# Optimization experiments

Measured on AMD Instinct MI355X. Metric: run time of the kernel, lower is better.

Reference implementation:

```python
import jax, jax.numpy as jnp
import numpy as np


def _ln(x, g, eps=1e-5):
    # channel LayerNorm over dim 1, unbiased=False variance
    mean = jnp.mean(x, axis=1, keepdims=True)
    var = jnp.mean((x - mean) ** 2, axis=1, keepdims=True)
    return (x - mean) * jax.lax.rsqrt(var + eps) * g


def _c11(x, w, b):
    # 1x1 conv: w (O,C), b (O,)
    return jnp.einsum('bchw,oc->bohw', x, w) + b[None, :, None, None]


def _dw(x, w, b):
    # depthwise 3x3 conv, SAME padding; w (C,1,3,3), b (C,)
    C = x.shape[1]
    y = jax.lax.conv_general_dilated(x, w, (1, 1), 'SAME',
                                     feature_group_count=C,
                                     dimension_numbers=('NCHW', 'OIHW', 'NCHW'))
    return y + b[None, :, None, None]


def _forward(F_i, F_w, g1, g2, qw1, qb1, kw1, kb1, vw1, vb1,
             qw2, qb2, kw2, kb2, vw2, vb2,
             qdw1, qdb1, kdw1, kdb1, vdw1, vdb1,
             qdw2, qdb2, kdw2, kdb2, vdw2, vdb2, lw, lb):
    B, C1, H, W = F_i.shape
    C2 = F_w.shape[1]
    HW = H * W
    fi = _ln(F_i, g1)
    fw = _ln(F_w, g2)
    # qkv = 1x1 conv -> depthwise conv; then RAW C-order reshape (torch .view)
    Qi = _dw(_c11(fi, qw1, qb1), qdw1, qdb1).reshape(B, HW, C1)
    Ki = _dw(_c11(fi, kw1, kb1), kdw1, kdb1).reshape(B, HW, C1)
    Vi = _dw(_c11(fi, vw1, vb1), vdw1, vdb1).reshape(B, C1, HW)
    Qw = _dw(_c11(fw, qw2, qb2), qdw2, qdb2).reshape(B, HW, C2)
    Kw = _dw(_c11(fw, kw2, kb2), kdw2, kdb2).reshape(B, HW, C2)
    Vw = _dw(_c11(fw, vw2, vb2), vdw2, vdb2).reshape(B, C2, HW)
    # channel cross-attention: (B,C1,HW)@(B,HW,C2) -> (B,C1,C2)
    a1 = jax.nn.softmax(jnp.einsum('bnc,bnd->bcd', Qi, Kw), axis=-1)
    a2 = jax.nn.softmax(jnp.einsum('bnc,bnd->bcd', Qw, Ki), axis=-1)
    Aw = jnp.einsum('bcd,bdn->bcn', a1, Vw).reshape(B, H, W, C2).transpose(0, 3, 1, 2)
    Ai = jnp.einsum('bcd,bdn->bcn', a2, Vi).reshape(B, H, W, C1).transpose(0, 3, 1, 2)
    cat = jnp.concatenate([Aw, Ai], axis=1)  # (B, C2+C1, H, W)
    Ct = cat.shape[1]
    flat = cat.reshape(B, Ct, HW).transpose(0, 2, 1).reshape(-1, Ct)  # (B*HW, Ct)
    out = flat @ lw.T + lb  # (B*HW, Cout)
    Cout = lb.shape[0]
    # faithful replication of torch's view/permute/view tail
    out = out.reshape(B, Cout, H, W).transpose(0, 2, 3, 1).reshape(B, Cout, H, W)
    return out + F_i + F_w


def setup_inputs() -> dict:
    key = jax.random.key(0)
    ks = jax.random.split(key, 20)
    B, C, H, W = 8, 128, 128, 128
    d = {}
    d['F_i'] = jax.random.normal(ks[0], (B, C, H, W), jnp.float32)
    d['F_w'] = jax.random.normal(ks[1], (B, C, H, W), jnp.float32)
    d['g1'] = jnp.ones((1, C, 1, 1), jnp.float32)
    d['g2'] = jnp.ones((1, C, 1, 1), jnp.float32)
    s = 1.0 / np.sqrt(C)
    i = 2
    for n in ['qw1', 'kw1', 'vw1', 'qw2', 'kw2', 'vw2']:
        d[n] = jax.random.normal(ks[i], (C, C), jnp.float32) * s
        i += 1
    for n in ['qb1', 'kb1', 'vb1', 'qb2', 'kb2', 'vb2']:
        d[n] = jnp.zeros((C,), jnp.float32)
    sd = 1.0 / 3.0
    for n in ['qdw1', 'kdw1', 'vdw1', 'qdw2', 'kdw2', 'vdw2']:
        d[n] = jax.random.normal(ks[i], (C, 1, 3, 3), jnp.float32) * sd
        i += 1
    for n in ['qdb1', 'kdb1', 'vdb1', 'qdb2', 'kdb2', 'vdb2']:
        d[n] = jnp.zeros((C,), jnp.float32)
    d['lw'] = jax.random.normal(ks[i], (C, 2 * C), jnp.float32) * (1.0 / np.sqrt(2 * C))
    d['lb'] = jnp.zeros((C,), jnp.float32)
    return d


def reference(F_i, F_w, g1, g2, qw1, qb1, kw1, kb1, vw1, vb1,
              qw2, qb2, kw2, kb2, vw2, vb2,
              qdw1, qdb1, kdw1, kdb1, vdw1, vdb1,
              qdw2, qdb2, kdw2, kdb2, vdw2, vdb2, lw, lb):
    return _forward(F_i, F_w, g1, g2, qw1, qb1, kw1, kb1, vw1, vb1,
                    qw2, qb2, kw2, kb2, vw2, vb2,
                    qdw1, qdb1, kdw1, kdb1, vdw1, vdb1,
                    qdw2, qdb2, kdw2, kdb2, vdw2, vdb2, lw, lb)
```

## Files before the change

kernel.cpp:

```cpp
#include <hip/hip_runtime.h>
#include <cstddef>
#include <cstring>

#define HW 16384
#define CC 128
#define NB 8
#define GB 4

typedef short bf16x8_t __attribute__((ext_vector_type(8)));
typedef float floatx4 __attribute__((ext_vector_type(4)));

__device__ inline unsigned short f2bf(float f) {
  unsigned u; __builtin_memcpy(&u, &f, 4);
  u += 0x7fffu + ((u >> 16) & 1u);
  return (unsigned short)(u >> 16);
}
__device__ inline float bf2f(unsigned short s) {
  unsigned u = ((unsigned)s) << 16; float f; __builtin_memcpy(&f, &u, 4);
  return f;
}

__global__ __launch_bounds__(256) void k_ln_stats(const float* __restrict__ x,
                                                  float* __restrict__ mean,
                                                  float* __restrict__ rstd) {
  int idx = blockIdx.x * 256 + threadIdx.x;
  int b = idx >> 14;
  int p = idx & (HW - 1);
  const float* xp = x + ((size_t)b << 21) + p;
  float s = 0.f, ss = 0.f;
  for (int c = 0; c < CC; ++c) {
    float v = xp[(size_t)c << 14];
    s += v;
    ss += v * v;
  }
  float m = s * (1.0f / CC);
  float var = ss * (1.0f / CC) - m * m;
  mean[idx] = m;
  rstd[idx] = rsqrtf(var + 1e-5f);
}

__global__ __launch_bounds__(256) void k_conv1x1_mfma(
    const float* __restrict__ X, const float* __restrict__ W,
    const float* __restrict__ bias, const float* __restrict__ g,
    const float* __restrict__ mean, const float* __restrict__ rstd,
    float* __restrict__ Y, int b0) {
  __shared__ __align__(16) float raw[32][132];
  __shared__ __align__(16) short Ah[128][40];
  __shared__ __align__(16) short Al[128][40];
  __shared__ __align__(16) short Bh[128][40];
  __shared__ __align__(16) short Bl[128][40];
  const int bl = blockIdx.y;
  const int b = b0 + bl;
  const int p0 = blockIdx.x * 128;
  const int t = threadIdx.x;
  const int lane = t & 63, wv = t >> 6;
  const int quad = lane >> 4, l15 = lane & 15;
  const int wr = wv >> 1, wc = wv & 1;

  const int s1c = t >> 3, s1p = (t & 7) * 16;
  const int sao = t >> 1, sas = (t & 1) * 16;
  const int s2p = t & 127, s2o = t >> 7;
  const float mu = mean[b * HW + p0 + s2p];
  const float rs = rstd[b * HW + p0 + s2p];

  const float* Xb = X + ((size_t)b << 21);
  floatx4 acc[4][4];
#pragma unroll
  for (int i = 0; i < 4; ++i)
#pragma unroll
    for (int j = 0; j < 4; ++j) acc[i][j] = (floatx4){0.f, 0.f, 0.f, 0.f};

  for (int k0 = 0; k0 < 128; k0 += 32) {
    {
      const float* xp = Xb + ((size_t)(k0 + s1c) << 14) + p0 + s1p;
#pragma unroll
      for (int u = 0; u < 4; ++u)
        *reinterpret_cast<float4*>(&raw[s1c][s1p + 4 * u]) =
            *reinterpret_cast<const float4*>(xp + 4 * u);
    }
    {
      const float* wp = W + sao * 128 + k0 + sas;
      const float* gp = g + k0 + sas;
      short th[16], tl[16];
#pragma unroll
      for (int j = 0; j < 16; ++j) {
        float v = wp[j] * gp[j];
        unsigned short h = f2bf(v);
        th[j] = (short)h;
        tl[j] = (short)f2bf(v - bf2f(h));
      }
#pragma unroll
      for (int j = 0; j < 2; ++j) {
        *reinterpret_cast<bf16x8_t*>(&Ah[sao][sas + 8 * j]) =
            *reinterpret_cast<bf16x8_t*>(&th[8 * j]);
        *reinterpret_cast<bf16x8_t*>(&Al[sao][sas + 8 * j]) =
            *reinterpret_cast<bf16x8_t*>(&tl[8 * j]);
      }
    }
    __syncthreads();
#pragma unroll
    for (int item = 0; item < 2; ++item) {
      const int oct = s2o + 2 * item;
      short th[8], tl[8];
#pragma unroll
      for (int jj = 0; jj < 8; ++jj) {
        float v = (raw[oct * 8 + jj][s2p] - mu) * rs;
        unsigned short h = f2bf(v);
        th[jj] = (short)h;
        tl[jj] = (short)f2bf(v - bf2f(h));
      }
      *reinterpret_cast<bf16x8_t*>(&Bh[s2p][oct * 8]) =
          *reinterpret_cast<bf16x8_t*>(&th[0]);
      *reinterpret_cast<bf16x8_t*>(&Bl[s2p][oct * 8]) =
          *reinterpret_cast<bf16x8_t*>(&tl[0]);
    }
    __syncthreads();
    bf16x8_t afh[4], afl[4], bfh[4], bfl[4];
#pragma unroll
    for (int i = 0; i < 4; ++i) {
      const int m = wr * 64 + i * 16 + l15;
      afh[i] = *reinterpret_cast<const bf16x8_t*>(&Ah[m][quad * 8]);
      afl[i] = *reinterpret_cast<const bf16x8_t*>(&Al[m][quad * 8]);
    }
#pragma unroll
    for (int j = 0; j < 4; ++j) {
      const int p = wc * 64 + j * 16 + l15;
      bfh[j] = *reinterpret_cast<const bf16x8_t*>(&Bh[p][quad * 8]);
      bfl[j] = *reinterpret_cast<const bf16x8_t*>(&Bl[p][quad * 8]);
    }
#pragma unroll
    for (int i = 0; i < 4; ++i)
#pragma unroll
      for (int j = 0; j < 4; ++j) {
        acc[i][j] = __builtin_amdgcn_mfma_f32_16x16x32_bf16(afh[i], bfh[j], acc[i][j], 0, 0, 0);
        acc[i][j] = __builtin_amdgcn_mfma_f32_16x16x32_bf16(afh[i], bfl[j], acc[i][j], 0, 0, 0);
        acc[i][j] = __builtin_amdgcn_mfma_f32_16x16x32_bf16(afl[i], bfh[j], acc[i][j], 0, 0, 0);
      }
    __syncthreads();
  }
  float* Yb = Y + ((size_t)bl << 21);
#pragma unroll
  for (int i = 0; i < 4; ++i) {
#pragma unroll
    for (int j = 0; j < 4; ++j) {
#pragma unroll
      for (int r = 0; r < 4; ++r) {
        const int o = wr * 64 + i * 16 + quad * 4 + r;
        const int p = p0 + wc * 64 + j * 16 + l15;
        Yb[((size_t)o << 14) + p] = acc[i][j][r] + bias[o];
      }
    }
  }
}

__global__ __launch_bounds__(256) void k_score_mfma(
    const float* __restrict__ Yq, const float* __restrict__ Yk,
    const float* __restrict__ qdw, const float* __restrict__ qdb,
    const float* __restrict__ kdw, const float* __restrict__ kdb,
    float* __restrict__ P) {
  __shared__ __align__(16) float raw[32][132];
  __shared__ __align__(16) short Ah[128][40];
  __shared__ __align__(16) short Al[128][40];
  __shared__ __align__(16) short Bh[128][40];
  __shared__ __align__(16) short Bl[128][40];
  const int ch = blockIdx.x;
  const int bl = blockIdx.y;
  const int t = threadIdx.x;
  const int lane = t & 63, wv = t >> 6;
  const int quad = lane >> 4, l15 = lane & 15;
  const int wr = wv >> 1, wc = wv & 1;
  const int h_loc = t >> 3;
  const int w0 = (t & 7) * 16;
  const int s2w = t & 127, s2o = t >> 7;
  const int cc = ch;
  const float* Yqb = Yq + ((size_t)bl << 21) + ((size_t)cc << 14);
  const float* Ykb = Yk + ((size_t)bl << 21) + ((size_t)cc << 14);
  const float* qwt = qdw + cc * 9;
  const float* kwt = kdw + cc * 9;
  const float qbv = qdb[cc], kbv = kdb[cc];

  floatx4 acc[4][4];
#pragma unroll
  for (int i = 0; i < 4; ++i)
#pragma unroll
    for (int j = 0; j < 4; ++j) acc[i][j] = (floatx4){0.f, 0.f, 0.f, 0.f};

  for (int k0 = 0; k0 < 128; k0 += 32) {
    const int h = k0 + h_loc;
#pragma unroll
    for (int side = 0; side < 2; ++side) {
      const float* Yc = side ? Ykb : Yqb;
      const float* wt = side ? kwt : qwt;
      const float bias = side ? kbv : qbv;
      float a[16];
#pragma unroll
      for (int j = 0; j < 16; ++j) a[j] = bias;
#pragma unroll
      for (int dy = 0; dy < 3; ++dy) {
        const int hh = h + dy - 1;
        if (hh < 0 || hh > 127) continue;
        const float* rp = Yc + (hh << 7) + w0;
        float4 f0 = *reinterpret_cast<const float4*>(rp);
        float4 f1 = *reinterpret_cast<const float4*>(rp + 4);
        float4 f2 = *reinterpret_cast<const float4*>(rp + 8);
        float4 f3 = *reinterpret_cast<const float4*>(rp + 12);
        float s[18];
        s[1] = f0.x;  s[2] = f0.y;  s[3] = f0.z;  s[4] = f0.w;
        s[5] = f1.x;  s[6] = f1.y;  s[7] = f1.z;  s[8] = f1.w;
        s[9] = f2.x;  s[10] = f2.y; s[11] = f2.z; s[12] = f2.w;
        s[13] = f3.x; s[14] = f3.y; s[15] = f3.z; s[16] = f3.w;
        s[0] = (w0 > 0) ? rp[-1] : 0.f;
        s[17] = (w0 < 112) ? rp[16] : 0.f;
        const float wa = wt[dy * 3 + 0], wb = wt[dy * 3 + 1], wc2 = wt[dy * 3 + 2];
#pragma unroll
        for (int j = 0; j < 16; ++j)
          a[j] = fmaf(s[j], wa, fmaf(s[j + 1], wb, fmaf(s[j + 2], wc2, a[j])));
      }
#pragma unroll
      for (int u = 0; u < 4; ++u)
        *reinterpret_cast<float4*>(&raw[h_loc][w0 + 4 * u]) =
            (float4){a[4 * u], a[4 * u + 1], a[4 * u + 2], a[4 * u + 3]};
      __syncthreads();
      short* dh = side ? &Bh[0][0] : &Ah[0][0];
      short* dl = side ? &Bl[0][0] : &Al[0][0];
#pragma unroll
      for (int item = 0; item < 2; ++item) {
        const int oct = s2o + 2 * item;
        short th[8], tl[8];
#pragma unroll
        for (int jj = 0; jj < 8; ++jj) {
          float v = raw[oct * 8 + jj][s2w];
          unsigned short hb = f2bf(v);
          th[jj] = (short)hb;
          tl[jj] = (short)f2bf(v - bf2f(hb));
        }
        *reinterpret_cast<bf16x8_t*>(&dh[s2w * 40 + oct * 8]) =
            *reinterpret_cast<bf16x8_t*>(&th[0]);
        *reinterpret_cast<bf16x8_t*>(&dl[s2w * 40 + oct * 8]) =
            *reinterpret_cast<bf16x8_t*>(&tl[0]);
      }
      __syncthreads();
    }
    bf16x8_t afh[4], afl[4], bfh[4], bfl[4];
#pragma unroll
    for (int i = 0; i < 4; ++i) {
      const int m = wr * 64 + i * 16 + l15;
      afh[i] = *reinterpret_cast<const bf16x8_t*>(&Ah[m][quad * 8]);
      afl[i] = *reinterpret_cast<const bf16x8_t*>(&Al[m][quad * 8]);
    }
#pragma unroll
    for (int j = 0; j < 4; ++j) {
      const int n = wc * 64 + j * 16 + l15;
      bfh[j] = *reinterpret_cast<const bf16x8_t*>(&Bh[n][quad * 8]);
      bfl[j] = *reinterpret_cast<const bf16x8_t*>(&Bl[n][quad * 8]);
    }
#pragma unroll
    for (int i = 0; i < 4; ++i)
#pragma unroll
      for (int j = 0; j < 4; ++j) {
        acc[i][j] = __builtin_amdgcn_mfma_f32_16x16x32_bf16(afh[i], bfh[j], acc[i][j], 0, 0, 0);
        acc[i][j] = __builtin_amdgcn_mfma_f32_16x16x32_bf16(afh[i], bfl[j], acc[i][j], 0, 0, 0);
        acc[i][j] = __builtin_amdgcn_mfma_f32_16x16x32_bf16(afl[i], bfh[j], acc[i][j], 0, 0, 0);
      }
  }
  float* Pp = P + ((size_t)(ch * GB + bl) << 14);
#pragma unroll
  for (int i = 0; i < 4; ++i) {
#pragma unroll
    for (int j = 0; j < 4; ++j) {
#pragma unroll
      for (int r = 0; r < 4; ++r) {
        const int c = wr * 64 + i * 16 + quad * 4 + r;
        const int d = wc * 64 + j * 16 + l15;
        Pp[c * 128 + d] = acc[i][j][r];
      }
    }
  }
}

__global__ __launch_bounds__(256) void k_score_reduce(const float* __restrict__ P,
                                                      float* __restrict__ S) {
  int idx = blockIdx.x * 256 + threadIdx.x;
  int bl = idx >> 14;
  int rem = idx & 16383;
  float s = 0.f;
  for (int c = 0; c < 128; ++c) s += P[((size_t)(c * GB + bl) << 14) + rem];
  S[idx] = s;
}

__global__ __launch_bounds__(128) void k_softmax(float* __restrict__ S) {
  __shared__ float red[128];
  const int row = blockIdx.x;
  const int t = threadIdx.x;
  float v = S[row * 128 + t];
  red[t] = v;
  __syncthreads();
  for (int s = 64; s > 0; s >>= 1) {
    if (t < s) red[t] = fmaxf(red[t], red[t + s]);
    __syncthreads();
  }
  float mx = red[0];
  __syncthreads();
  float e = expf(v - mx);
  red[t] = e;
  __syncthreads();
  for (int s = 64; s > 0; s >>= 1) {
    if (t < s) red[t] += red[t + s];
    __syncthreads();
  }
  S[row * 128 + t] = e / red[0];
}

__global__ __launch_bounds__(256) void k_dw_t(const float* __restrict__ Y,
                                              const float* __restrict__ Kw,
                                              const float* __restrict__ db,
                                              unsigned short* __restrict__ Vt) {
  __shared__ unsigned short T[128][33];
  const int h = blockIdx.x;
  const int c0 = blockIdx.y * 32;
  const int bl = blockIdx.z;
  const int t = threadIdx.x;
  const int cl = t >> 3;
  const int w0 = (t & 7) * 16;
  const int c = c0 + cl;
  const float* Yc = Y + ((size_t)bl << 21) + ((size_t)c << 14);
  const float* wt = Kw + c * 9;
  float a[16];
#pragma unroll
  for (int j = 0; j < 16; ++j) a[j] = db[c];
#pragma unroll
  for (int dy = 0; dy < 3; ++dy) {
    const int hh = h + dy - 1;
    if (hh < 0 || hh > 127) continue;
    const float* rp = Yc + (hh << 7) + w0;
    float4 f0 = *reinterpret_cast<const float4*>(rp);
    float4 f1 = *reinterpret_cast<const float4*>(rp + 4);
    float4 f2 = *reinterpret_cast<const float4*>(rp + 8);
    float4 f3 = *reinterpret_cast<const float4*>(rp + 12);
    float s[18];
    s[1] = f0.x;  s[2] = f0.y;  s[3] = f0.z;  s[4] = f0.w;
    s[5] = f1.x;  s[6] = f1.y;  s[7] = f1.z;  s[8] = f1.w;
    s[9] = f2.x;  s[10] = f2.y; s[11] = f2.z; s[12] = f2.w;
    s[13] = f3.x; s[14] = f3.y; s[15] = f3.z; s[16] = f3.w;
    s[0] = (w0 > 0) ? rp[-1] : 0.f;
    s[17] = (w0 < 112) ? rp[16] : 0.f;
    const float wa = wt[dy * 3 + 0], wb = wt[dy * 3 + 1], wc2 = wt[dy * 3 + 2];
#pragma unroll
    for (int j = 0; j < 16; ++j)
      a[j] = fmaf(s[j], wa, fmaf(s[j + 1], wb, fmaf(s[j + 2], wc2, a[j])));
  }
#pragma unroll
  for (int j = 0; j < 16; ++j) T[w0 + j][cl] = f2bf(a[j]);
  __syncthreads();
  const int w = t >> 1, half = t & 1;
  unsigned short tmp[16];
#pragma unroll
  for (int j = 0; j < 16; ++j) tmp[j] = T[w][half * 16 + j];
  uint4 v0, v1;
  unsigned* vp0 = reinterpret_cast<unsigned*>(&v0);
  unsigned* vp1 = reinterpret_cast<unsigned*>(&v1);
#pragma unroll
  for (int j = 0; j < 4; ++j) {
    vp0[j] = (unsigned)tmp[2 * j] | ((unsigned)tmp[2 * j + 1] << 16);
    vp1[j] = (unsigned)tmp[8 + 2 * j] | ((unsigned)tmp[8 + 2 * j + 1] << 16);
  }
  unsigned short* dst = Vt + ((size_t)bl << 21) + ((size_t)((h << 7) + w) << 7)
                        + c0 + half * 16;
  *reinterpret_cast<uint4*>(dst) = v0;
  *reinterpret_cast<uint4*>(dst + 8) = v1;
}

__global__ __launch_bounds__(256) void k_av_mfma(
    const float* __restrict__ S, const unsigned short* __restrict__ Vt,
    unsigned short* __restrict__ O) {
  __shared__ __align__(16) short As[128][136];
  const int bl = blockIdx.y;
  const int p0 = blockIdx.x * 128;
  const int t = threadIdx.x;
  const int lane = t & 63, wv = t >> 6;
  const int quad = lane >> 4, l15 = lane & 15;
  const int wr = wv >> 1, wc = wv & 1;
  {
    const float* Ab = S + ((size_t)bl << 14);
    const int r = t >> 1, hf = (t & 1) * 64;
    const float* src = Ab + r * 128 + hf;
    short tmp[64];
#pragma unroll
    for (int j = 0; j < 64; ++j) tmp[j] = (short)f2bf(src[j]);
#pragma unroll
    for (int j = 0; j < 8; ++j)
      *reinterpret_cast<bf16x8_t*>(&As[r][hf + j * 8]) =
          *reinterpret_cast<bf16x8_t*>(&tmp[j * 8]);
  }
  __syncthreads();
  floatx4 acc[4][4];
#pragma unroll
  for (int i = 0; i < 4; ++i)
#pragma unroll
    for (int j = 0; j < 4; ++j) acc[i][j] = (floatx4){0.f, 0.f, 0.f, 0.f};
  const unsigned short* Vb = Vt + ((size_t)bl << 21);
#pragma unroll
  for (int d0 = 0; d0 < 128; d0 += 32) {
    bf16x8_t af[4], bf[4];
#pragma unroll
    for (int i = 0; i < 4; ++i) {
      const int m = wr * 64 + i * 16 + l15;
      af[i] = *reinterpret_cast<const bf16x8_t*>(&As[m][d0 + quad * 8]);
    }
#pragma unroll
    for (int j = 0; j < 4; ++j) {
      const int p = p0 + wc * 64 + j * 16 + l15;
      bf[j] = *reinterpret_cast<const bf16x8_t*>(Vb + ((size_t)p << 7) + d0 + quad * 8);
    }
#pragma unroll
    for (int i = 0; i < 4; ++i)
#pragma unroll
      for (int j = 0; j < 4; ++j)
        acc[i][j] = __builtin_amdgcn_mfma_f32_16x16x32_bf16(af[i], bf[j], acc[i][j], 0, 0, 0);
  }
  unsigned short* Ob = O + ((size_t)bl << 21);
#pragma unroll
  for (int i = 0; i < 4; ++i) {
#pragma unroll
    for (int j = 0; j < 4; ++j) {
#pragma unroll
      for (int r = 0; r < 4; ++r) {
        const int c = wr * 64 + i * 16 + quad * 4 + r;
        const int p = p0 + wc * 64 + j * 16 + l15;
        Ob[((size_t)c << 14) + p] = f2bf(acc[i][j][r]);
      }
    }
  }
}

__global__ __launch_bounds__(256) void k_final2_mfma(
    const unsigned short* __restrict__ A1, const unsigned short* __restrict__ A2,
    const float* __restrict__ lw, const float* __restrict__ lb,
    const float* __restrict__ Fi, const float* __restrict__ Fw,
    float* __restrict__ out, int b0) {
  __shared__ __align__(16) short As[128][136];
  const int c2 = blockIdx.x;
  const int bl = blockIdx.y;
  const int b = b0 + bl;
  const int t = threadIdx.x;
  const int lane = t & 63, wv = t >> 6;
  const int quad = lane >> 4, l15 = lane & 15;
  const int wr = wv >> 1, wc = wv & 1;
  floatx4 acc[4][4];
#pragma unroll
  for (int i = 0; i < 4; ++i)
#pragma unroll
    for (int j = 0; j < 4; ++j) acc[i][j] = (floatx4){0.f, 0.f, 0.f, 0.f};
#pragma unroll
  for (int phase = 0; phase < 2; ++phase) {
    {
      const int r = t >> 1, hf = (t & 1) * 64;
      const float* src = lw + r * 256 + phase * 128 + hf;
      short tmp[64];
#pragma unroll
      for (int j = 0; j < 64; ++j) tmp[j] = (short)f2bf(src[j]);
#pragma unroll
      for (int j = 0; j < 8; ++j)
        *reinterpret_cast<bf16x8_t*>(&As[r][hf + j * 8]) =
            *reinterpret_cast<bf16x8_t*>(&tmp[j * 8]);
    }
    __syncthreads();
    const unsigned short* Ub = (phase ? A2 : A1) + ((size_t)bl << 21) + c2 * 128;
#pragma unroll
    for (int d0 = 0; d0 < 128; d0 += 32) {
      bf16x8_t af[4], bf[4];
#pragma unroll
      for (int i = 0; i < 4; ++i) {
        const int m = wr * 64 + i * 16 + l15;
        af[i] = *reinterpret_cast<const bf16x8_t*>(&As[m][d0 + quad * 8]);
      }
#pragma unroll
      for (int j = 0; j < 4; ++j) {
        const int n = wc * 64 + j * 16 + l15;
        bf[j] = *reinterpret_cast<const bf16x8_t*>(Ub + ((size_t)n << 14) + d0 + quad * 8);
      }
#pragma unroll
      for (int i = 0; i < 4; ++i)
#pragma unroll
        for (int j = 0; j < 4; ++j)
          acc[i][j] = __builtin_amdgcn_mfma_f32_16x16x32_bf16(af[i], bf[j], acc[i][j], 0, 0, 0);
    }
    __syncthreads();
  }
  const size_t obase = ((size_t)b << 21) + ((size_t)c2 << 14);
#pragma unroll
  for (int i = 0; i < 4; ++i) {
#pragma unroll
    for (int j = 0; j < 4; ++j) {
#pragma unroll
      for (int r = 0; r < 4; ++r) {
        const int h2 = wr * 64 + i * 16 + quad * 4 + r;
        const int w2 = wc * 64 + j * 16 + l15;
        const size_t a = obase + ((size_t)h2 << 7) + w2;
        out[a] = acc[i][j][r] + lb[h2] + Fi[a] + Fw[a];
      }
    }
  }
}

extern "C" void kernel_launch(void* const* d_in, const int* in_sizes, int n_in,
                              void* d_out, int out_size, void* d_ws, size_t ws_size,
                              hipStream_t stream) {
  const float* F_i  = (const float*)d_in[0];
  const float* F_w  = (const float*)d_in[1];
  const float* g1   = (const float*)d_in[2];
  const float* g2   = (const float*)d_in[3];
  const float* qw1  = (const float*)d_in[4];
  const float* kw1  = (const float*)d_in[5];
  const float* vw1  = (const float*)d_in[6];
  const float* qw2  = (const float*)d_in[7];
  const float* kw2  = (const float*)d_in[8];
  const float* vw2  = (const float*)d_in[9];
  const float* qb1  = (const float*)d_in[10];
  const float* kb1  = (const float*)d_in[11];
  const float* vb1  = (const float*)d_in[12];
  const float* qb2  = (const float*)d_in[13];
  const float* kb2  = (const float*)d_in[14];
  const float* vb2  = (const float*)d_in[15];
  const float* qdw1 = (const float*)d_in[16];
  const float* kdw1 = (const float*)d_in[17];
  const float* vdw1 = (const float*)d_in[18];
  const float* qdw2 = (const float*)d_in[19];
  const float* kdw2 = (const float*)d_in[20];
  const float* vdw2 = (const float*)d_in[21];
  const float* qdb1 = (const float*)d_in[22];
  const float* kdb1 = (const float*)d_in[23];
  const float* vdb1 = (const float*)d_in[24];
  const float* qdb2 = (const float*)d_in[25];
  const float* kdb2 = (const float*)d_in[26];
  const float* vdb2 = (const float*)d_in[27];
  const float* lw   = (const float*)d_in[28];
  const float* lb   = (const float*)d_in[29];
  float* out = (float*)d_out;

  char* w = (char*)d_ws;
  const size_t NTOT = (size_t)NB * HW;
  float* meanI = (float*)w; w += NTOT * 4;
  float* rstdI = (float*)w; w += NTOT * 4;
  float* meanW = (float*)w; w += NTOT * 4;
  float* rstdW = (float*)w; w += NTOT * 4;
  float* S     = (float*)w; w += (size_t)GB * HW * 4;
  float* P     = (float*)w; w += (size_t)128 * GB * HW * 4;
  float* Yq    = (float*)w; w += ((size_t)GB << 21) * 4;
  char*  Ykreg = w;         w += ((size_t)GB << 21) * 4;
  float* Yk    = (float*)Ykreg;
  unsigned short* Vt = (unsigned short*)Ykreg;
  unsigned short* A2 = (unsigned short*)(Ykreg + ((size_t)GB << 21) * 2);
  unsigned short* A1 = (unsigned short*)w; w += ((size_t)GB << 21) * 2;

  dim3 blk(256);
  k_ln_stats<<<dim3(512), blk, 0, stream>>>(F_i, meanI, rstdI);
  k_ln_stats<<<dim3(512), blk, 0, stream>>>(F_w, meanW, rstdW);

  for (int b0 = 0; b0 < NB; b0 += GB) {
    k_conv1x1_mfma<<<dim3(128, GB), blk, 0, stream>>>(F_i, qw1, qb1, g1, meanI, rstdI, Yq, b0);
    k_conv1x1_mfma<<<dim3(128, GB), blk, 0, stream>>>(F_w, kw2, kb2, g2, meanW, rstdW, Yk, b0);
    k_score_mfma<<<dim3(128, GB), blk, 0, stream>>>(Yq, Yk, qdw1, qdb1, kdw2, kdb2, P);
    k_score_reduce<<<dim3(GB * HW / 256), blk, 0, stream>>>(P, S);
    k_softmax<<<dim3(GB * 128), dim3(128), 0, stream>>>(S);
    k_conv1x1_mfma<<<dim3(128, GB), blk, 0, stream>>>(F_w, vw2, vb2, g2, meanW, rstdW, Yq, b0);
    k_dw_t<<<dim3(128, 4, GB), blk, 0, stream>>>(Yq, vdw2, vdb2, Vt);
    k_av_mfma<<<dim3(128, GB), blk, 0, stream>>>(S, Vt, A1);

    k_conv1x1_mfma<<<dim3(128, GB), blk, 0, stream>>>(F_w, qw2, qb2, g2, meanW, rstdW, Yq, b0);
    k_conv1x1_mfma<<<dim3(128, GB), blk, 0, stream>>>(F_i, kw1, kb1, g1, meanI, rstdI, Yk, b0);
    k_score_mfma<<<dim3(128, GB), blk, 0, stream>>>(Yq, Yk, qdw2, qdb2, kdw1, kdb1, P);
    k_score_reduce<<<dim3(GB * HW / 256), blk, 0, stream>>>(P, S);
    k_softmax<<<dim3(GB * 128), dim3(128), 0, stream>>>(S);
    k_conv1x1_mfma<<<dim3(128, GB), blk, 0, stream>>>(F_i, vw1, vb1, g1, meanI, rstdI, Yq, b0);
    k_dw_t<<<dim3(128, 4, GB), blk, 0, stream>>>(Yq, vdw1, vdb1, Vt);
    k_av_mfma<<<dim3(128, GB), blk, 0, stream>>>(S, Vt, A2);

    k_final2_mfma<<<dim3(128, GB), blk, 0, stream>>>(A1, A2, lw, lb, F_i, F_w, out, b0);
  }
}
```

Before: 838.9 us.

## Precompute split-bf16 weights once and read MFMA A-operands from global

A new kernel converts the six gamma-scaled 1x1 conv weights into hi/lo bf16 pairs and the linear weight into bf16, once per call. The conv1x1 and final kernels then read these A fragments straight from global memory instead of converting them into shared memory in every block. k_av and k_final also halve their tile width to double the grid and drop their shared-memory staging. k_score shrinks its raw buffer and processes 16-row sub-tiles, which adds extra barriers. The cost is that A fragments are now fetched from global or L2 by every wave, with no shared-memory reuse.

Result: slower. 893.1 us (+6.5%).

```diff
diff --git a/kernel.cpp b/kernel.cpp
--- a/kernel.cpp
+++ b/kernel.cpp
@@ -39,16 +39,46 @@
   rstd[idx] = rsqrtf(var + 1e-5f);
 }
 
+__global__ __launch_bounds__(256) void k_wsplit(
+    const float* __restrict__ qw1, const float* __restrict__ kw2,
+    const float* __restrict__ vw2, const float* __restrict__ qw2,
+    const float* __restrict__ kw1, const float* __restrict__ vw1,
+    const float* __restrict__ g1, const float* __restrict__ g2,
+    const float* __restrict__ lw, unsigned short* __restrict__ whl,
+    unsigned short* __restrict__ lwh) {
+  int idx = blockIdx.x * 256 + threadIdx.x;
+  if (idx < 98304) {
+    const int set = idx >> 14;
+    const int e = idx & 16383;
+    const int c = e & 127;
+    const float* W; const float* g;
+    switch (set) {
+      case 0: W = qw1; g = g1; break;
+      case 1: W = kw2; g = g2; break;
+      case 2: W = vw2; g = g2; break;
+      case 3: W = qw2; g = g2; break;
+      case 4: W = kw1; g = g1; break;
+      default: W = vw1; g = g1; break;
+    }
+    float v = W[e] * g[c];
+    unsigned short h = f2bf(v);
+    whl[set * 32768 + e] = h;
+    whl[set * 32768 + 16384 + e] = f2bf(v - bf2f(h));
+  } else {
+    int e2 = idx - 98304;
+    lwh[e2] = f2bf(lw[e2]);
+  }
+}
+
 __global__ __launch_bounds__(256) void k_conv1x1_mfma(
-    const float* __restrict__ X, const float* __restrict__ W,
-    const float* __restrict__ bias, const float* __restrict__ g,
+    const float* __restrict__ X, const unsigned short* __restrict__ Wh,
+    const float* __restrict__ bias,
     const float* __restrict__ mean, const float* __restrict__ rstd,
     float* __restrict__ Y, int b0) {
   __shared__ __align__(16) float raw[32][132];
-  __shared__ __align__(16) short Ah[128][40];
-  __shared__ __align__(16) short Al[128][40];
   __shared__ __align__(16) short Bh[128][40];
   __shared__ __align__(16) short Bl[128][40];
+  const unsigned short* Wl = Wh + 16384;
   const int bl = blockIdx.y;
   const int b = b0 + bl;
   const int p0 = blockIdx.x * 128;
@@ -58,7 +88,6 @@
   const int wr = wv >> 1, wc = wv & 1;
 
   const int s1c = t >> 3, s1p = (t & 7) * 16;
-  const int sao = t >> 1, sas = (t & 1) * 16;
   const int s2p = t & 127, s2o = t >> 7;
   const float mu = mean[b * HW + p0 + s2p];
   const float rs = rstd[b * HW + p0 + s2p];
@@ -77,25 +106,6 @@
       for (int u = 0; u < 4; ++u)
         *reinterpret_cast<float4*>(&raw[s1c][s1p + 4 * u]) =
             *reinterpret_cast<const float4*>(xp + 4 * u);
-    }
-    {
-      const float* wp = W + sao * 128 + k0 + sas;
-      const float* gp = g + k0 + sas;
-      short th[16], tl[16];
-#pragma unroll
-      for (int j = 0; j < 16; ++j) {
-        float v = wp[j] * gp[j];
-        unsigned short h = f2bf(v);
-        th[j] = (short)h;
-        tl[j] = (short)f2bf(v - bf2f(h));
-      }
-#pragma unroll
-      for (int j = 0; j < 2; ++j) {
-        *reinterpret_cast<bf16x8_t*>(&Ah[sao][sas + 8 * j]) =
-            *reinterpret_cast<bf16x8_t*>(&th[8 * j]);
-        *reinterpret_cast<bf16x8_t*>(&Al[sao][sas + 8 * j]) =
-            *reinterpret_cast<bf16x8_t*>(&tl[8 * j]);
-      }
     }
     __syncthreads();
 #pragma unroll
@@ -119,8 +129,9 @@
 #pragma unroll
     for (int i = 0; i < 4; ++i) {
       const int m = wr * 64 + i * 16 + l15;
-      afh[i] = *reinterpret_cast<const bf16x8_t*>(&Ah[m][quad * 8]);
-      afl[i] = *reinterpret_cast<const bf16x8_t*>(&Al[m][quad * 8]);
+      const unsigned short* wp = Wh + m * 128 + k0 + quad * 8;
+      afh[i] = *reinterpret_cast<const bf16x8_t*>(wp);
+      afl[i] = *reinterpret_cast<const bf16x8_t*>(Wl + m * 128 + k0 + quad * 8);
     }
 #pragma unroll
     for (int j = 0; j < 4; ++j) {
@@ -158,7 +169,7 @@
     const float* __restrict__ qdw, const float* __restrict__ qdb,
     const float* __restrict__ kdw, const float* __restrict__ kdb,
     float* __restrict__ P) {
-  __shared__ __align__(16) float raw[32][132];
+  __shared__ __align__(16) float raw[16][132];
   __shared__ __align__(16) short Ah[128][40];
   __shared__ __align__(16) short Al[128][40];
   __shared__ __align__(16) short Bh[128][40];
@@ -169,8 +180,8 @@
   const int lane = t & 63, wv = t >> 6;
   const int quad = lane >> 4, l15 = lane & 15;
   const int wr = wv >> 1, wc = wv & 1;
-  const int h_loc = t >> 3;
-  const int w0 = (t & 7) * 16;
+  const int hl = t >> 4;
+  const int w0 = (t & 15) * 8;
   const int s2w = t & 127, s2o = t >> 7;
   const int cc = ch;
   const float* Yqb = Yq + ((size_t)bl << 21) + ((size_t)cc << 14);
@@ -186,60 +197,53 @@
     for (int j = 0; j < 4; ++j) acc[i][j] = (floatx4){0.f, 0.f, 0.f, 0.f};
 
   for (int k0 = 0; k0 < 128; k0 += 32) {
-    const int h = k0 + h_loc;
 #pragma unroll
     for (int side = 0; side < 2; ++side) {
       const float* Yc = side ? Ykb : Yqb;
       const float* wt = side ? kwt : qwt;
       const float bias = side ? kbv : qbv;
-      float a[16];
-#pragma unroll
-      for (int j = 0; j < 16; ++j) a[j] = bias;
-#pragma unroll
-      for (int dy = 0; dy < 3; ++dy) {
-        const int hh = h + dy - 1;
-        if (hh < 0 || hh > 127) continue;
-        const float* rp = Yc + (hh << 7) + w0;
-        float4 f0 = *reinterpret_cast<const float4*>(rp);
-        float4 f1 = *reinterpret_cast<const float4*>(rp + 4);
-        float4 f2 = *reinterpret_cast<const float4*>(rp + 8);
-        float4 f3 = *reinterpret_cast<const float4*>(rp + 12);
-        float s[18];
-        s[1] = f0.x;  s[2] = f0.y;  s[3] = f0.z;  s[4] = f0.w;
-        s[5] = f1.x;  s[6] = f1.y;  s[7] = f1.z;  s[8] = f1.w;
-        s[9] = f2.x;  s[10] = f2.y; s[11] = f2.z; s[12] = f2.w;
-        s[13] = f3.x; s[14] = f3.y; s[15] = f3.z; s[16] = f3.w;
-        s[0] = (w0 > 0) ? rp[-1] : 0.f;
-        s[17] = (w0 < 112) ? rp[16] : 0.f;
-        const float wa = wt[dy * 3 + 0], wb = wt[dy * 3 + 1], wc2 = wt[dy * 3 + 2];
-#pragma unroll
-        for (int j = 0; j < 16; ++j)
-          a[j] = fmaf(s[j], wa, fmaf(s[j + 1], wb, fmaf(s[j + 2], wc2, a[j])));
-      }
-#pragma unroll
-      for (int u = 0; u < 4; ++u)
-        *reinterpret_cast<float4*>(&raw[h_loc][w0 + 4 * u]) =
-            (float4){a[4 * u], a[4 * u + 1], a[4 * u + 2], a[4 * u + 3]};
-      __syncthreads();
       short* dh = side ? &Bh[0][0] : &Ah[0][0];
       short* dl = side ? &Bl[0][0] : &Al[0][0];
 #pragma unroll
-      for (int item = 0; item < 2; ++item) {
-        const int oct = s2o + 2 * item;
+      for (int sub = 0; sub < 2; ++sub) {
+        const int h = k0 + sub * 16 + hl;
+        float a[8];
+#pragma unroll
+        for (int j = 0; j < 8; ++j) a[j] = bias;
+#pragma unroll
+        for (int dy = 0; dy < 3; ++dy) {
+          const int hh = h + dy - 1;
+          if (hh < 0 || hh > 127) continue;
+          const float* rp = Yc + (hh << 7) + w0;
+          float4 f0 = *reinterpret_cast<const float4*>(rp);
+          float4 f1 = *reinterpret_cast<const float4*>(rp + 4);
+          float v[10];
+          v[0] = (w0 > 0) ? rp[-1] : 0.f;
+          v[1] = f0.x; v[2] = f0.y; v[3] = f0.z; v[4] = f0.w;
+          v[5] = f1.x; v[6] = f1.y; v[7] = f1.z; v[8] = f1.w;
+          v[9] = (w0 < 120) ? rp[8] : 0.f;
+          const float wa = wt[dy * 3 + 0], wb = wt[dy * 3 + 1], wc2 = wt[dy * 3 + 2];
+#pragma unroll
+          for (int j = 0; j < 8; ++j)
+            a[j] = fmaf(v[j], wa, fmaf(v[j + 1], wb, fmaf(v[j + 2], wc2, a[j])));
+        }
+        *reinterpret_cast<float4*>(&raw[hl][w0]) = (float4){a[0], a[1], a[2], a[3]};
+        *reinterpret_cast<float4*>(&raw[hl][w0 + 4]) = (float4){a[4], a[5], a[6], a[7]};
+        __syncthreads();
         short th[8], tl[8];
 #pragma unroll
         for (int jj = 0; jj < 8; ++jj) {
-          float v = raw[oct * 8 + jj][s2w];
+          float v = raw[s2o * 8 + jj][s2w];
           unsigned short hb = f2bf(v);
           th[jj] = (short)hb;
           tl[jj] = (short)f2bf(v - bf2f(hb));
         }
-        *reinterpret_cast<bf16x8_t*>(&dh[s2w * 40 + oct * 8]) =
+        *reinterpret_cast<bf16x8_t*>(&dh[s2w * 40 + sub * 16 + s2o * 8]) =
             *reinterpret_cast<bf16x8_t*>(&th[0]);
-        *reinterpret_cast<bf16x8_t*>(&dl[s2w * 40 + oct * 8]) =
+        *reinterpret_cast<bf16x8_t*>(&dl[s2w * 40 + sub * 16 + s2o * 8]) =
             *reinterpret_cast<bf16x8_t*>(&tl[0]);
-      }
-      __syncthreads();
+        __syncthreads();
+      }
     }
     bf16x8_t afh[4], afl[4], bfh[4], bfl[4];
 #pragma unroll
@@ -373,60 +377,55 @@
 __global__ __launch_bounds__(256) void k_av_mfma(
     const float* __restrict__ S, const unsigned short* __restrict__ Vt,
     unsigned short* __restrict__ O) {
-  __shared__ __align__(16) short As[128][136];
   const int bl = blockIdx.y;
-  const int p0 = blockIdx.x * 128;
+  const int p0 = blockIdx.x * 64;
   const int t = threadIdx.x;
   const int lane = t & 63, wv = t >> 6;
   const int quad = lane >> 4, l15 = lane & 15;
   const int wr = wv >> 1, wc = wv & 1;
-  {
-    const float* Ab = S + ((size_t)bl << 14);
-    const int r = t >> 1, hf = (t & 1) * 64;
-    const float* src = Ab + r * 128 + hf;
-    short tmp[64];
-#pragma unroll
-    for (int j = 0; j < 64; ++j) tmp[j] = (short)f2bf(src[j]);
-#pragma unroll
-    for (int j = 0; j < 8; ++j)
-      *reinterpret_cast<bf16x8_t*>(&As[r][hf + j * 8]) =
-          *reinterpret_cast<bf16x8_t*>(&tmp[j * 8]);
-  }
-  __syncthreads();
-  floatx4 acc[4][4];
+  const float* Sb = S + ((size_t)bl << 14);
+  floatx4 acc[4][2];
 #pragma unroll
   for (int i = 0; i < 4; ++i)
 #pragma unroll
-    for (int j = 0; j < 4; ++j) acc[i][j] = (floatx4){0.f, 0.f, 0.f, 0.f};
+    for (int j = 0; j < 2; ++j) acc[i][j] = (floatx4){0.f, 0.f, 0.f, 0.f};
   const unsigned short* Vb = Vt + ((size_t)bl << 21);
 #pragma unroll
   for (int d0 = 0; d0 < 128; d0 += 32) {
-    bf16x8_t af[4], bf[4];
+    bf16x8_t af[4], bf[2];
 #pragma unroll
     for (int i = 0; i < 4; ++i) {
       const int m = wr * 64 + i * 16 + l15;
-      af[i] = *reinterpret_cast<const bf16x8_t*>(&As[m][d0 + quad * 8]);
-    }
-#pragma unroll
-    for (int j = 0; j < 4; ++j) {
-      const int p = p0 + wc * 64 + j * 16 + l15;
+      const float* sp = Sb + m * 128 + d0 + quad * 8;
+      float4 x0 = *reinterpret_cast<const float4*>(sp);
+      float4 x1 = *reinterpret_cast<const float4*>(sp + 4);
+      short tmp[8];
+      tmp[0] = (short)f2bf(x0.x); tmp[1] = (short)f2bf(x0.y);
+      tmp[2] = (short)f2bf(x0.z); tmp[3] = (short)f2bf(x0.w);
+      tmp[4] = (short)f2bf(x1.x); tmp[5] = (short)f2bf(x1.y);
+      tmp[6] = (short)f2bf(x1.z); tmp[7] = (short)f2bf(x1.w);
+      af[i] = *reinterpret_cast<bf16x8_t*>(&tmp[0]);
+    }
+#pragma unroll
+    for (int j = 0; j < 2; ++j) {
+      const int p = p0 + wc * 32 + j * 16 + l15;
       bf[j] = *reinterpret_cast<const bf16x8_t*>(Vb + ((size_t)p << 7) + d0 + quad * 8);
     }
 #pragma unroll
     for (int i = 0; i < 4; ++i)
 #pragma unroll
-      for (int j = 0; j < 4; ++j)
+      for (int j = 0; j < 2; ++j)
         acc[i][j] = __builtin_amdgcn_mfma_f32_16x16x32_bf16(af[i], bf[j], acc[i][j], 0, 0, 0);
   }
   unsigned short* Ob = O + ((size_t)bl << 21);
 #pragma unroll
   for (int i = 0; i < 4; ++i) {
 #pragma unroll
-    for (int j = 0; j < 4; ++j) {
+    for (int j = 0; j < 2; ++j) {
 #pragma unroll
       for (int r = 0; r < 4; ++r) {
         const int c = wr * 64 + i * 16 + quad * 4 + r;
-        const int p = p0 + wc * 64 + j * 16 + l15;
+        const int p = p0 + wc * 32 + j * 16 + l15;
         Ob[((size_t)c << 14) + p] = f2bf(acc[i][j][r]);
       }
     }
@@ -435,67 +434,55 @@
 
 __global__ __launch_bounds__(256) void k_final2_mfma(
     const unsigned short* __restrict__ A1, const unsigned short* __restrict__ A2,
-    const float* __restrict__ lw, const float* __restrict__ lb,
+    const unsigned short* __restrict__ lwh, const float* __restrict__ lb,
     const float* __restrict__ Fi, const float* __restrict__ Fw,
     float* __restrict__ out, int b0) {
-  __shared__ __align__(16) short As[128][136];
   const int c2 = blockIdx.x;
   const int bl = blockIdx.y;
+  const int nb = blockIdx.z * 64;
   const int b = b0 + bl;
   const int t = threadIdx.x;
   const int lane = t & 63, wv = t >> 6;
   const int quad = lane >> 4, l15 = lane & 15;
   const int wr = wv >> 1, wc = wv & 1;
-  floatx4 acc[4][4];
+  floatx4 acc[4][2];
 #pragma unroll
   for (int i = 0; i < 4; ++i)
 #pragma unroll
-    for (int j = 0; j < 4; ++j) acc[i][j] = (floatx4){0.f, 0.f, 0.f, 0.f};
+    for (int j = 0; j < 2; ++j) acc[i][j] = (floatx4){0.f, 0.f, 0.f, 0.f};
 #pragma unroll
   for (int phase = 0; phase < 2; ++phase) {
-    {
-      const int r = t >> 1, hf = (t & 1) * 64;
-      const float* src = lw + r * 256 + phase * 128 + hf;
-      short tmp[64];
-#pragma unroll
-      for (int j = 0; j < 64; ++j) tmp[j] = (short)f2bf(src[j]);
-#pragma unroll
-      for (int j = 0; j < 8; ++j)
-        *reinterpret_cast<bf16x8_t*>(&As[r][hf + j * 8]) =
-            *reinterpret_cast<bf16x8_t*>(&tmp[j * 8]);
-    }
-    __syncthreads();
     const unsigned short* Ub = (phase ? A2 : A1) + ((size_t)bl << 21) + c2 * 128;
 #pragma unroll
     for (int d0 = 0; d0 < 128; d0 += 32) {
-      bf16x8_t af[4], bf[4];
+      bf16x8_t af[4], bf[2];
 #pragma unroll
       for (int i = 0; i < 4; ++i) {
         const int m = wr * 64 + i * 16 + l15;
-        af[i] = *reinterpret_cast<const bf16x8_t*>(&As[m][d0 + quad * 8]);
-      }
-#pragma unroll
-      for (int j = 0; j < 4; ++j) {
-        const int n = wc * 64 + j * 16 + l15;
+        af[i] = *reinterpret_cast<const bf16x8_t*>(
+            lwh + m * 256 + phase * 128 + d0 + quad * 8);
+      }
+#pragma unroll
+      for (int j = 0; j < 2; ++j) {
+        const int n = nb + wc * 32 + j * 16 + l15;
         bf[j] = *reinterpret_cast<const bf16x8_t*>(Ub + ((size_t)n << 14) + d0 + quad * 8);
       }
 #pragma unroll
       for (int i = 0; i < 4; ++i)
 #pragma unroll
-        for (int j = 0; j < 4; ++j)
+        for (int j = 0; j < 2; ++j)
           acc[i][j] = __builtin_amdgcn_mfma_f32_16x16x32_bf16(af[i], bf[j], acc[i][j], 0, 0, 0);
     }
-    __syncthreads();
   }
   const size_t obase = ((size_t)b << 21) + ((size_t)c2 << 14);
 #pragma unroll
   for (int i = 0; i < 4; ++i) {
 #pragma unroll
-    for (int j = 0; j < 4; ++j) {
+    for (int j = 0; j < 2; ++j) {
 #pragma unroll
       for (int r = 0; r < 4; ++r) {
         const int h2 = wr * 64 + i * 16 + quad * 4 + r;
-        const int w2 = wc * 64 + j * 16 + l15;
+        const int w2 = nb + wc * 32 + j * 16 + l15;
         const size_t a = obase + ((size_t)h2 << 7) + w2;
         out[a] = acc[i][j][r] + lb[h2] + Fi[a] + Fw[a];
       }
@@ -545,6 +532,8 @@
   float* meanW = (float*)w; w += NTOT * 4;
   float* rstdW = (float*)w; w += NTOT * 4;
   float* S     = (float*)w; w += (size_t)GB * HW * 4;
+  unsigned short* whl = (unsigned short*)w; w += 6 * 32768 * 2;
+  unsigned short* lwh = (unsigned short*)w; w += 32768 * 2;
   float* P     = (float*)w; w += (size_t)128 * GB * HW * 4;
   float* Yq    = (float*)w; w += ((size_t)GB << 21) * 4;
   char*  Ykreg = w;         w += ((size_t)GB << 21) * 4;
@@ -556,26 +545,34 @@
   dim3 blk(256);
   k_ln_stats<<<dim3(512), blk, 0, stream>>>(F_i, meanI, rstdI);
   k_ln_stats<<<dim3(512), blk, 0, stream>>>(F_w, meanW, rstdW);
+  k_wsplit<<<dim3(512), blk, 0, stream>>>(qw1, kw2, vw2, qw2, kw1, vw1,
+                                          g1, g2, lw, whl, lwh);
+  const unsigned short* wQ1 = whl;
+  const unsigned short* wK2 = whl + 32768;
+  const unsigned short* wV2 = whl + 65536;
+  const unsigned short* wQ2 = whl + 98304;
+  const unsigned short* wK1 = whl + 131072;
+  const unsigned short* wV1 = whl + 163840;
 
   for (int b0 = 0; b0 < NB; b0 += GB) {
-    k_conv1x1_mfma<<<dim3(128, GB), blk, 0, stream>>>(F_i, qw1, qb1, g1, meanI, rstdI, Yq, b0);
-    k_conv1x1_mfma<<<dim3(128, GB), blk, 0, stream>>>(F_w, kw2, kb2, g2, meanW, rstdW, Yk, b0);
+    k_conv1x1_mfma<<<dim3(128, GB), blk, 0, stream>>>(F_i, wQ1, qb1, meanI, rstdI, Yq, b0);
+    k_conv1x1_mfma<<<dim3(128, GB), blk, 0, stream>>>(F_w, wK2, kb2, meanW, rstdW, Yk, b0);
     k_score_mfma<<<dim3(128, GB), blk, 0, stream>>>(Yq, Yk, qdw1, qdb1, kdw2, kdb2, P);
     k_score_reduce<<<dim3(GB * HW / 256), blk, 0, stream>>>(P, S);
     k_softmax<<<dim3(GB * 128), dim3(128), 0, stream>>>(S);
-    k_conv1x1_mfma<<<dim3(128, GB), blk, 0, stream>>>(F_w, vw2, vb2, g2, meanW, rstdW, Yq, b0);
+    k_conv1x1_mfma<<<dim3(128, GB), blk, 0, stream>>>(F_w, wV2, vb2, meanW, rstdW, Yq, b0);
     k_dw_t<<<dim3(128, 4, GB), blk, 0, stream>>>(Yq, vdw2, vdb2, Vt);
-    k_av_mfma<<<dim3(128, GB), blk, 0, stream>>>(S, Vt, A1);
-
-    k_conv1x1_mfma<<<dim3(128, GB), blk, 0, stream>>>(F_w, qw2, qb2, g2, meanW, rstdW, Yq, b0);
-    k_conv1x1_mfma<<<dim3(128, GB), blk, 0, stream>>>(F_i, kw1, kb1, g1, meanI, rstdI, Yk, b0);
+    k_av_mfma<<<dim3(256, GB), blk, 0, stream>>>(S, Vt, A1);
+
+    k_conv1x1_mfma<<<dim3(128, GB), blk, 0, stream>>>(F_w, wQ2, qb2, meanW, rstdW, Yq, b0);
+    k_conv1x1_mfma<<<dim3(128, GB), blk, 0, stream>>>(F_i, wK1, kb1, meanI, rstdI, Yk, b0);
     k_score_mfma<<<dim3(128, GB), blk, 0, stream>>>(Yq, Yk, qdw2, qdb2, kdw1, kdb1, P);
     k_score_reduce<<<dim3(GB * HW / 256), blk, 0, stream>>>(P, S);
     k_softmax<<<dim3(GB * 128), dim3(128), 0, stream>>>(S);
-    k_conv1x1_mfma<<<dim3(128, GB), blk, 0, stream>>>(F_i, vw1, vb1, g1, meanI, rstdI, Yq, b0);
+    k_conv1x1_mfma<<<dim3(128, GB), blk, 0, stream>>>(F_i, wV1, vb1, meanI, rstdI, Yq, b0);
     k_dw_t<<<dim3(128, 4, GB), blk, 0, stream>>>(Yq, vdw1, vdb1, Vt);
-    k_av_mfma<<<dim3(128, GB), blk, 0, stream>>>(S, Vt, A2);
-
-    k_final2_mfma<<<dim3(128, GB), blk, 0, stream>>>(A1, A2, lw, lb, F_i, F_w, out, b0);
-  }
-}
+    k_av_mfma<<<dim3(256, GB), blk, 0, stream>>>(S, Vt, A2);
+
+    k_final2_mfma<<<dim3(128, GB, 2), blk, 0, stream>>>(A1, A2, lwh, lb, F_i, F_w, out, b0);
+  }
+}
```
